# Kernel optimization log

Measured on AMD Instinct MI355X. Metric: run time of the kernel, lower is better.

Reference implementation:

```python
import jax, jax.numpy as jnp
import numpy as np

T, D, F, E, K = 2048, 512, 2048, 8, 2


def setup_inputs() -> dict:
    key = jax.random.key(0)
    ks = jax.random.split(key, 5)
    scaled = lambda k, shape, fan: jax.random.normal(k, shape, jnp.float32) * (fan ** -0.5)
    x = jax.random.normal(ks[0], (T, D), jnp.float32)
    Wg = scaled(ks[1], (D, E), D)          # gate: Linear(D -> E), no bias
    W1 = scaled(ks[2], (E, D, F), D)       # per-expert up proj
    W3 = scaled(ks[3], (E, D, F), D)       # per-expert gate proj (SwiGLU)
    W2 = scaled(ks[4], (E, F, D), F)       # per-expert down proj
    return {"x": x, "Wg": Wg, "W1": W1, "W2": W2, "W3": W3}


def reference(x, Wg, W1, W2, W3):
    # gate logits + top-k routing (topk over raw logits, softmax over the k picked logits,
    # computed in float32 then cast back -- matches the torch source)
    logits = x @ Wg                                   # [T, E]
    topw, sel = jax.lax.top_k(logits, K)              # [T, K] each
    weights = jax.nn.softmax(topw.astype(jnp.float32), axis=-1).astype(x.dtype)
    out = jnp.zeros_like(x)
    # NOTE: the source uses `output[batch_idx] = ...` (assignment, not +=), so later
    # experts OVERWRITE earlier ones for tokens routed to multiple experts.
    # We replicate that exactly with sequential jnp.where overwrites.
    for i in range(E):
        hit = sel == i                                # [T, K]
        mask = hit.any(axis=-1)                       # [T] tokens routed to expert i
        w_i = jnp.sum(jnp.where(hit, weights, 0.0), axis=-1)  # [T] routing weight
        h = jax.nn.silu(x @ W1[i]) * (x @ W3[i])      # [T, F] SwiGLU
        y = h @ W2[i]                                 # [T, D]
        out = jnp.where(mask[:, None], w_i[:, None] * y, out)
    return out
```

## Files before the change

kernel.cpp:

```cpp
#include <hip/hip_runtime.h>
#include <hip/hip_bf16.h>
#include <math.h>

typedef __attribute__((ext_vector_type(8))) short short8;
typedef __attribute__((ext_vector_type(4))) float f32x4;

#define T_TOK 2048
#define D_DIM 512
#define F_DIM 2048
#define E_NUM 8
#define MAXT1 40

__device__ __forceinline__ unsigned short f2bf(float f) {
  union { float f; unsigned u; } c; c.f = f;
  unsigned u = c.u;
  return (unsigned short)((u + 0x7fffu + ((u >> 16) & 1u)) >> 16);
}

__device__ __forceinline__ void gld16(const void* g, void* l) {
  __builtin_amdgcn_global_load_lds((const __attribute__((address_space(1))) int*)g,
                                   (__attribute__((address_space(3))) int*)l, 16, 0, 0);
}

__global__ __launch_bounds__(256) void k_prep(const float* __restrict__ xin,
                                              const float* __restrict__ Wg,
                                              const float* __restrict__ W1,
                                              const float* __restrict__ W3,
                                              int* __restrict__ jbuf,
                                              float* __restrict__ wbuf,
                                              unsigned short* __restrict__ xb,
                                              unsigned short* __restrict__ w1f,
                                              unsigned short* __restrict__ w3f) {
  __shared__ float4 tile4[64 * 32];
  int bz = blockIdx.x, tid = threadIdx.x;

  if (bz < 256) {
    int gid = bz * 256 + tid;
    int t = gid >> 5, seg = gid & 31;
    const float* xp = xin + (size_t)t * D_DIM + seg * 16;
    unsigned short* xo = xb + (size_t)t * D_DIM + seg * 16;
    float acc[8];
#pragma unroll
    for (int e = 0; e < 8; ++e) acc[e] = 0.f;
#pragma unroll
    for (int i = 0; i < 4; ++i) {
      float4 v = *(const float4*)(xp + i * 4);
      ushort4 o;
      o.x = f2bf(v.x); o.y = f2bf(v.y); o.z = f2bf(v.z); o.w = f2bf(v.w);
      *(ushort4*)(xo + i * 4) = o;
      const float* xs = (const float*)&v;
#pragma unroll
      for (int q = 0; q < 4; ++q) {
        int d = seg * 16 + i * 4 + q;
        const float4* wr = (const float4*)(Wg + (size_t)d * 8);
        float4 w0 = wr[0], w1 = wr[1];
        acc[0] += xs[q] * w0.x; acc[1] += xs[q] * w0.y;
        acc[2] += xs[q] * w0.z; acc[3] += xs[q] * w0.w;
        acc[4] += xs[q] * w1.x; acc[5] += xs[q] * w1.y;
        acc[6] += xs[q] * w1.z; acc[7] += xs[q] * w1.w;
      }
    }
#pragma unroll
    for (int off = 1; off < 32; off <<= 1)
#pragma unroll
      for (int e = 0; e < 8; ++e) acc[e] += __shfl_xor(acc[e], off);
    if (seg == 0) {
      float l0 = -1e30f, l1 = -1e30f; int i0 = 0, i1 = 0;
#pragma unroll
      for (int e = 0; e < 8; ++e) {
        float l = acc[e];
        if (l > l0) { l1 = l0; i1 = i0; l0 = l; i0 = e; }
        else if (l > l1) { l1 = l; i1 = e; }
      }
      int j; float w;
      if (i0 > i1) { j = i0; w = 1.f / (1.f + expf(l1 - l0)); }
      else         { j = i1; w = 1.f / (1.f + expf(l0 - l1)); }
      jbuf[t] = j; wbuf[t] = w;
    }
    return;
  }

  int idx = bz - 256;
  int z = idx >> 7, rem = idx & 127;
  const int K = 512, N = 2048;
  int n0 = (rem & 15) * 128, k0 = (rem >> 4) * 64;
  size_t zsz = (size_t)(K / 32) * (N / 16) * 512;
  const float* in; unsigned short* out;
  if (z < 8) { in = W1 + (size_t)z * K * N;       out = w1f + (size_t)z * zsz; }
  else       { in = W3 + (size_t)(z - 8) * K * N; out = w3f + (size_t)(z - 8) * zsz; }
  {
    int lr = tid >> 5, lc = tid & 31;
#pragma unroll
    for (int it = 0; it < 8; ++it) {
      int row = it * 8 + lr;
      float4 v = *(const float4*)(in + (size_t)(k0 + row) * N + n0 + lc * 4);
      tile4[row * 32 + ((lc + (row >> 3) * 4) & 31)] = v;
    }
  }
  __syncthreads();
  const float* tf = (const float*)tile4;
  int wv = tid >> 6, l = tid & 63;
  int n4l = (l & 15) >> 2, nr = l & 3, kg = (l >> 4) * 8;
#pragma unroll
  for (int q = 0; q < 4; ++q) {
    int fid = wv * 4 + q;
    int nb = fid >> 1, kb = fid & 1;
    int n4 = nb * 4 + n4l;
    short8 o;
#pragma unroll
    for (int j = 0; j < 8; ++j) {
      int k = kb * 32 + kg + j;
      int slot = k * 32 + ((n4 + (k >> 3) * 4) & 31);
      o[j] = (short)f2bf(tf[slot * 4 + nr]);
    }
    unsigned short* op = out + (((size_t)(n0 / 16 + nb) * (K / 32)) + (k0 / 32 + kb)) * 512 + l * 8;
    *(short8*)op = o;
  }
}

__global__ __launch_bounds__(256) void k_bucket(const int* __restrict__ jbuf,
                                                int* __restrict__ cntp,
                                                int* __restrict__ basep,
                                                int* __restrict__ list,
                                                int* __restrict__ tl1,
                                                int* __restrict__ ntl) {
  __shared__ int scnt[8], scur[8];
  int tid = threadIdx.x;
  if (tid < 8) scnt[tid] = 0;
  __syncthreads();
  for (int t = tid; t < T_TOK; t += 256) atomicAdd(&scnt[jbuf[t]], 1);
  __syncthreads();
  if (tid == 0) {
    int run = 0;
    for (int e = 0; e < 8; ++e) {
      cntp[e] = scnt[e]; basep[e] = run; scur[e] = run;
      run += scnt[e];
    }
    int n1 = 0, bb = 0;
    for (int e = 0; e < 8; ++e) {
      for (int m = 0; m < scnt[e]; m += 64) tl1[n1++] = (e << 16) | (bb + m);
      bb += scnt[e];
    }
    ntl[0] = n1;
  }
  __syncthreads();
  for (int t = tid; t < T_TOK; t += 256) {
    int j = jbuf[t];
    int p = atomicAdd(&scur[j], 1);
    list[p] = t;
  }
}

__global__ __launch_bounds__(256, 2) void k_ffn1w2(const unsigned short* __restrict__ xb,
                                                   const unsigned short* __restrict__ w1f,
                                                   const unsigned short* __restrict__ w3f,
                                                   const float* __restrict__ W2,
                                                   unsigned short* __restrict__ w2f,
                                                   const int* __restrict__ cntp,
                                                   const int* __restrict__ basep,
                                                   const int* __restrict__ list,
                                                   const int* __restrict__ tl1,
                                                   const int* __restrict__ ntl,
                                                   unsigned short* __restrict__ hbuf) {
  __shared__ unsigned short sA[64 * 512];
  int tid = threadIdx.x, wv = tid >> 6, l = tid & 63;

  if (blockIdx.x >= 640) {
    int idx = blockIdx.x - 640;
    int z = idx >> 7, rem = idx & 127;
    const int K = 2048, N = 512;
    int n0 = (rem & 3) * 128, k0 = (rem >> 2) * 64;
    size_t zsz = (size_t)(K / 32) * (N / 16) * 512;
    const float* in = W2 + (size_t)z * K * N;
    unsigned short* out = w2f + (size_t)z * zsz;
    float4* tile4 = (float4*)sA;
    {
      int lr = tid >> 5, lc = tid & 31;
#pragma unroll
      for (int it = 0; it < 8; ++it) {
        int row = it * 8 + lr;
        float4 v = *(const float4*)(in + (size_t)(k0 + row) * N + n0 + lc * 4);
        tile4[row * 32 + ((lc + (row >> 3) * 4) & 31)] = v;
      }
    }
    __syncthreads();
    const float* tf = (const float*)tile4;
    int n4l = (l & 15) >> 2, nr = l & 3, kg = (l >> 4) * 8;
#pragma unroll
    for (int q = 0; q < 4; ++q) {
      int fid = wv * 4 + q;
      int nb = fid >> 1, kb = fid & 1;
      int n4 = nb * 4 + n4l;
      short8 o;
#pragma unroll
      for (int j = 0; j < 8; ++j) {
        int k = kb * 32 + kg + j;
        int slot = k * 32 + ((n4 + (k >> 3) * 4) & 31);
        o[j] = (short)f2bf(tf[slot * 4 + nr]);
      }
      unsigned short* op = out + (((size_t)(n0 / 16 + nb) * (K / 32)) + (k0 / 32 + kb)) * 512 + l * 8;
      *(short8*)op = o;
    }
    return;
  }

  int L = blockIdx.x;
  int b = (L & 7) * 80 + (L >> 3);
  int x = b % 40, y = b / 40;
  if (x >= ntl[0]) return;
  int pk = tl1[x];
  int e = pk >> 16, g0 = pk & 0xffff;
  int lim = basep[e] + cntp[e];
  int wr = wv >> 1, wc = wv & 1;

#pragma unroll
  for (int it = 0; it < 16; ++it) {
    int row = wv * 16 + it;
    int gr = g0 + row; if (gr >= lim) gr = lim - 1;
    int tok = list[gr];
    int slot = (l & 56) | ((l & 7) ^ (row & 7));
    gld16(xb + (size_t)tok * D_DIM + slot * 8, sA + row * 512);
  }

  const unsigned short* w1b = w1f + ((size_t)(e * 128 + y * 8 + wc) * 16) * 512 + l * 8;
  const unsigned short* w3b = w3f + ((size_t)(e * 128 + y * 8 + wc) * 16) * 512 + l * 8;

  short8 P1[8], P3[8], Q1[8], Q3[8];
  auto loadS = [&](short8* r1, short8* r3, int s) {
    int g = s >> 1, h = s & 1;
    const unsigned short* p1 = w1b + ((size_t)(g * 32 + h * 8)) * 512;
    const unsigned short* p3 = w3b + ((size_t)(g * 32 + h * 8)) * 512;
#pragma unroll
    for (int q = 0; q < 8; ++q) {
      r1[q] = *(const short8*)(p1 + (size_t)q * 512);
      r3[q] = *(const short8*)(p3 + (size_t)q * 512);
    }
  };

  f32x4 au[2], av[2];
  auto halfC = [&](const short8* r1, const short8* r3, int h) {
#pragma unroll
    for (int q = 0; q < 8; ++q) {
      int kf = h * 8 + q;
      short8 a[2];
#pragma unroll
      for (int i = 0; i < 2; ++i) {
        int r = wr * 32 + i * 16 + (l & 15);
        int slot = kf * 4 + (l >> 4);
        int swz = (slot & 56) | ((slot & 7) ^ (r & 7));
        a[i] = *(const short8*)(sA + r * 512 + swz * 8);
      }
#pragma unroll
      for (int i = 0; i < 2; ++i) {
        au[i] = __builtin_amdgcn_mfma_f32_16x16x32_bf16(a[i], r1[q], au[i], 0, 0, 0);
        av[i] = __builtin_amdgcn_mfma_f32_16x16x32_bf16(a[i], r3[q], av[i], 0, 0, 0);
      }
    }
  };

  loadS(P1, P3, 0);
  __syncthreads();

  int cloc = l & 15, rb = (l >> 4) * 4;
#pragma unroll
  for (int gp = 0; gp < 4; ++gp) {
#pragma unroll
    for (int i = 0; i < 2; ++i) {
      au[i] = (f32x4){0.f, 0.f, 0.f, 0.f};
      av[i] = (f32x4){0.f, 0.f, 0.f, 0.f};
    }
    loadS(Q1, Q3, gp * 2 + 1);
    halfC(P1, P3, 0);
    if (gp < 3) loadS(P1, P3, gp * 2 + 2);
    halfC(Q1, Q3, 1);
    int col = (y * 4 + gp) * 32 + wc * 16 + cloc;
#pragma unroll
    for (int i = 0; i < 2; ++i)
#pragma unroll
      for (int r = 0; r < 4; ++r) {
        int gr = g0 + wr * 32 + i * 16 + rb + r;
        if (gr < lim) {
          float uu = au[i][r], vv = av[i][r];
          float hh = (uu / (1.f + expf(-uu))) * vv;
          hbuf[(size_t)gr * F_DIM + col] = f2bf(hh);
        }
      }
  }
}

__global__ __launch_bounds__(256, 3) void k_ffn2(const unsigned short* __restrict__ hbuf,
                                                 const unsigned short* __restrict__ w2f,
                                                 const int* __restrict__ cntp,
                                                 const int* __restrict__ basep,
                                                 const int* __restrict__ list,
                                                 const int* __restrict__ tl1,
                                                 const int* __restrict__ ntl,
                                                 const float* __restrict__ wbuf,
                                                 float* __restrict__ out) {
  int L = blockIdx.x;
  int c = L & 7, q = L >> 3;
  int x = c * 5 + (q % 5);
  int nt = q / 5;
  if (x >= ntl[0]) return;
  int pk = tl1[x];
  int e = pk >> 16, g0 = pk & 0xffff;
  int lim = basep[e] + cntp[e];
  __shared__ unsigned short sA[2 * 8192];
  int tid = threadIdx.x, wv = tid >> 6, l = tid & 63;
  int wr = wv >> 1, wc = wv & 1;

  auto stage = [&](int buf, int ck) {
#pragma unroll
    for (int it = 0; it < 4; ++it) {
      int row0 = it * 16 + wv * 4;
      int row = row0 + (l >> 4);
      int gr = g0 + row; if (gr > T_TOK - 1) gr = T_TOK - 1;
      int sl = (l & 8) | ((l & 7) ^ (row & 7));
      gld16(hbuf + (size_t)gr * F_DIM + ck * 128 + sl * 8, sA + buf * 8192 + row0 * 128);
    }
  };

  const unsigned short* b2p = w2f + ((size_t)(e * 32 + nt * 2 + wc) * 64) * 512 + l * 8;

  short8 Ba[4], Bb[4];
  auto loadB = [&](short8* B, int ck) {
#pragma unroll
    for (int kk = 0; kk < 4; ++kk)
      B[kk] = *(const short8*)(b2p + (size_t)(ck * 4 + kk) * 512);
  };

  f32x4 acc[2];
  acc[0] = (f32x4){0.f, 0.f, 0.f, 0.f};
  acc[1] = (f32x4){0.f, 0.f, 0.f, 0.f};

  auto compute = [&](const short8* B, int cur) {
#pragma unroll
    for (int kk = 0; kk < 4; ++kk) {
      short8 a[2];
#pragma unroll
      for (int i = 0; i < 2; ++i) {
        int r = wr * 32 + i * 16 + (l & 15);
        int slot = kk * 4 + (l >> 4);
        int swz = (slot & 8) | ((slot & 7) ^ (r & 7));
        a[i] = *(const short8*)(sA + cur * 8192 + r * 128 + swz * 8);
      }
      acc[0] = __builtin_amdgcn_mfma_f32_16x16x32_bf16(a[0], B[kk], acc[0], 0, 0, 0);
      acc[1] = __builtin_amdgcn_mfma_f32_16x16x32_bf16(a[1], B[kk], acc[1], 0, 0, 0);
    }
  };

  stage(0, 0);
  loadB(Ba, 0);
  __syncthreads();
  int cur = 0;
  for (int ck = 0; ck < 16; ck += 2) {
    stage(cur ^ 1, ck + 1);
    loadB(Bb, ck + 1);
    compute(Ba, cur);
    __syncthreads();
    cur ^= 1;
    if (ck + 2 < 16) {
      stage(cur ^ 1, ck + 2);
      loadB(Ba, ck + 2);
    }
    compute(Bb, cur);
    __syncthreads();
    cur ^= 1;
  }

  int cloc = l & 15, rb = (l >> 4) * 4;
#pragma unroll
  for (int i = 0; i < 2; ++i)
#pragma unroll
    for (int r = 0; r < 4; ++r) {
      int gr = g0 + wr * 32 + i * 16 + rb + r;
      if (gr < lim) {
        int tok = list[gr];
        out[(size_t)tok * D_DIM + nt * 32 + wc * 16 + cloc] = wbuf[tok] * acc[i][r];
      }
    }
}

extern "C" void kernel_launch(void* const* d_in, const int* in_sizes, int n_in,
                              void* d_out, int out_size, void* d_ws, size_t ws_size,
                              hipStream_t stream) {
  const float* x  = (const float*)d_in[0];
  const float* Wg = (const float*)d_in[1];
  const float* W1 = (const float*)d_in[2];
  const float* W2 = (const float*)d_in[3];
  const float* W3 = (const float*)d_in[4];
  float* out = (float*)d_out;
  char* ws = (char*)d_ws;

  int*            jbuf  = (int*)(ws + 0);
  float*          wbuf  = (float*)(ws + 8192);
  int*            cntp  = (int*)(ws + 16384);
  int*            basep = (int*)(ws + 16448);
  int*            list  = (int*)(ws + 16640);
  int*            tl1   = (int*)(ws + 24832);
  int*            ntl   = (int*)(ws + 25600);
  unsigned short* xb    = (unsigned short*)(ws + 32768);
  unsigned short* w1f   = (unsigned short*)(ws + 32768 + 2097152);
  unsigned short* w3f   = (unsigned short*)(ws + 32768 + 2097152 + 16777216);
  unsigned short* w2f   = (unsigned short*)(ws + 32768 + 2097152 + 2 * 16777216);
  unsigned short* hbuf  = (unsigned short*)(ws + 32768 + 2097152 + 3 * 16777216);

  k_prep<<<dim3(2304), dim3(256), 0, stream>>>(x, Wg, W1, W3, jbuf, wbuf, xb, w1f, w3f);
  k_bucket<<<dim3(1), dim3(256), 0, stream>>>(jbuf, cntp, basep, list, tl1, ntl);
  k_ffn1w2<<<dim3(1664), dim3(256), 0, stream>>>(xb, w1f, w3f, W2, w2f, cntp, basep, list, tl1, ntl, hbuf);
  k_ffn2<<<dim3(640), dim3(256), 0, stream>>>(hbuf, w2f, cntp, basep, list, tl1, ntl, wbuf, out);
}
```

Before: 79.82 us.

## Split routing kernel, fuse bucketing into weight prep, double-buffer weight conversion tiles

Routing and x-to-bf16 conversion move into their own kernel. The single-block bucketing kernel is folded in as an extra block of the W1/W3 conversion kernel, so bucketing runs alongside weight conversion instead of as a separate serial launch. Each weight-conversion block now handles two 64-row k tiles with a double-buffered LDS tile, which halves the block count and overlaps the next tile's loads with the current tile's conversion and stores. The cost is more LDS per block in prep2, which may lower occupancy.

```diff
diff --git a/kernel.cpp b/kernel.cpp
--- a/kernel.cpp
+++ b/kernel.cpp
@@ -22,133 +22,141 @@
                                    (__attribute__((address_space(3))) int*)l, 16, 0, 0);
 }
 
-__global__ __launch_bounds__(256) void k_prep(const float* __restrict__ xin,
-                                              const float* __restrict__ Wg,
-                                              const float* __restrict__ W1,
-                                              const float* __restrict__ W3,
-                                              int* __restrict__ jbuf,
-                                              float* __restrict__ wbuf,
-                                              unsigned short* __restrict__ xb,
-                                              unsigned short* __restrict__ w1f,
-                                              unsigned short* __restrict__ w3f) {
-  __shared__ float4 tile4[64 * 32];
+__global__ __launch_bounds__(256) void k_route(const float* __restrict__ xin,
+                                               const float* __restrict__ Wg,
+                                               int* __restrict__ jbuf,
+                                               float* __restrict__ wbuf,
+                                               unsigned short* __restrict__ xb) {
+  int gid = blockIdx.x * 256 + threadIdx.x;
+  int t = gid >> 5, seg = gid & 31;
+  const float* xp = xin + (size_t)t * D_DIM + seg * 16;
+  unsigned short* xo = xb + (size_t)t * D_DIM + seg * 16;
+  float acc[8];
+#pragma unroll
+  for (int e = 0; e < 8; ++e) acc[e] = 0.f;
+#pragma unroll
+  for (int i = 0; i < 4; ++i) {
+    float4 v = *(const float4*)(xp + i * 4);
+    ushort4 o;
+    o.x = f2bf(v.x); o.y = f2bf(v.y); o.z = f2bf(v.z); o.w = f2bf(v.w);
+    *(ushort4*)(xo + i * 4) = o;
+    const float* xs = (const float*)&v;
+#pragma unroll
+    for (int q = 0; q < 4; ++q) {
+      int d = seg * 16 + i * 4 + q;
+      const float4* wr = (const float4*)(Wg + (size_t)d * 8);
+      float4 w0 = wr[0], w1 = wr[1];
+      acc[0] += xs[q] * w0.x; acc[1] += xs[q] * w0.y;
+      acc[2] += xs[q] * w0.z; acc[3] += xs[q] * w0.w;
+      acc[4] += xs[q] * w1.x; acc[5] += xs[q] * w1.y;
+      acc[6] += xs[q] * w1.z; acc[7] += xs[q] * w1.w;
+    }
+  }
+#pragma unroll
+  for (int off = 1; off < 32; off <<= 1)
+#pragma unroll
+    for (int e = 0; e < 8; ++e) acc[e] += __shfl_xor(acc[e], off);
+  if (seg == 0) {
+    float l0 = -1e30f, l1 = -1e30f; int i0 = 0, i1 = 0;
+#pragma unroll
+    for (int e = 0; e < 8; ++e) {
+      float l = acc[e];
+      if (l > l0) { l1 = l0; i1 = i0; l0 = l; i0 = e; }
+      else if (l > l1) { l1 = l; i1 = e; }
+    }
+    int j; float w;
+    if (i0 > i1) { j = i0; w = 1.f / (1.f + expf(l1 - l0)); }
+    else         { j = i1; w = 1.f / (1.f + expf(l0 - l1)); }
+    jbuf[t] = j; wbuf[t] = w;
+  }
+}
+
+__global__ __launch_bounds__(256) void k_prep2(const float* __restrict__ W1,
+                                               const float* __restrict__ W3,
+                                               unsigned short* __restrict__ w1f,
+                                               unsigned short* __restrict__ w3f,
+                                               const int* __restrict__ jbuf,
+                                               int* __restrict__ cntp,
+                                               int* __restrict__ basep,
+                                               int* __restrict__ list,
+                                               int* __restrict__ tl1,
+                                               int* __restrict__ ntl) {
+  __shared__ float4 tile4[2][64 * 32];
+  __shared__ int scnt[8], scur[8];
   int bz = blockIdx.x, tid = threadIdx.x;
 
-  if (bz < 256) {
-    int gid = bz * 256 + tid;
-    int t = gid >> 5, seg = gid & 31;
-    const float* xp = xin + (size_t)t * D_DIM + seg * 16;
-    unsigned short* xo = xb + (size_t)t * D_DIM + seg * 16;
-    float acc[8];
-#pragma unroll
-    for (int e = 0; e < 8; ++e) acc[e] = 0.f;
-#pragma unroll
-    for (int i = 0; i < 4; ++i) {
-      float4 v = *(const float4*)(xp + i * 4);
-      ushort4 o;
-      o.x = f2bf(v.x); o.y = f2bf(v.y); o.z = f2bf(v.z); o.w = f2bf(v.w);
-      *(ushort4*)(xo + i * 4) = o;
-      const float* xs = (const float*)&v;
-#pragma unroll
-      for (int q = 0; q < 4; ++q) {
-        int d = seg * 16 + i * 4 + q;
-        const float4* wr = (const float4*)(Wg + (size_t)d * 8);
-        float4 w0 = wr[0], w1 = wr[1];
-        acc[0] += xs[q] * w0.x; acc[1] += xs[q] * w0.y;
-        acc[2] += xs[q] * w0.z; acc[3] += xs[q] * w0.w;
-        acc[4] += xs[q] * w1.x; acc[5] += xs[q] * w1.y;
-        acc[6] += xs[q] * w1.z; acc[7] += xs[q] * w1.w;
-      }
-    }
-#pragma unroll
-    for (int off = 1; off < 32; off <<= 1)
-#pragma unroll
-      for (int e = 0; e < 8; ++e) acc[e] += __shfl_xor(acc[e], off);
-    if (seg == 0) {
-      float l0 = -1e30f, l1 = -1e30f; int i0 = 0, i1 = 0;
-#pragma unroll
+  if (bz >= 1024) {
+    if (tid < 8) scnt[tid] = 0;
+    __syncthreads();
+    for (int t = tid; t < T_TOK; t += 256) atomicAdd(&scnt[jbuf[t]], 1);
+    __syncthreads();
+    if (tid == 0) {
+      int run = 0;
       for (int e = 0; e < 8; ++e) {
-        float l = acc[e];
-        if (l > l0) { l1 = l0; i1 = i0; l0 = l; i0 = e; }
-        else if (l > l1) { l1 = l; i1 = e; }
-      }
-      int j; float w;
-      if (i0 > i1) { j = i0; w = 1.f / (1.f + expf(l1 - l0)); }
-      else         { j = i1; w = 1.f / (1.f + expf(l0 - l1)); }
-      jbuf[t] = j; wbuf[t] = w;
+        cntp[e] = scnt[e]; basep[e] = run; scur[e] = run;
+        run += scnt[e];
+      }
+      int n1 = 0, bb = 0;
+      for (int e = 0; e < 8; ++e) {
+        for (int m = 0; m < scnt[e]; m += 64) tl1[n1++] = (e << 16) | (bb + m);
+        bb += scnt[e];
+      }
+      ntl[0] = n1;
+    }
+    __syncthreads();
+    for (int t = tid; t < T_TOK; t += 256) {
+      int j = jbuf[t];
+      int p = atomicAdd(&scur[j], 1);
+      list[p] = t;
     }
     return;
   }
 
-  int idx = bz - 256;
-  int z = idx >> 7, rem = idx & 127;
+  int z = bz >> 6, rem = bz & 63;
   const int K = 512, N = 2048;
-  int n0 = (rem & 15) * 128, k0 = (rem >> 4) * 64;
+  int n0 = (rem & 15) * 128, k0 = (rem >> 4) * 128;
   size_t zsz = (size_t)(K / 32) * (N / 16) * 512;
   const float* in; unsigned short* out;
   if (z < 8) { in = W1 + (size_t)z * K * N;       out = w1f + (size_t)z * zsz; }
   else       { in = W3 + (size_t)(z - 8) * K * N; out = w3f + (size_t)(z - 8) * zsz; }
-  {
-    int lr = tid >> 5, lc = tid & 31;
+
+  int lr = tid >> 5, lc = tid & 31;
+  int wv = tid >> 6, l = tid & 63;
+  int n4l = (l & 15) >> 2, nr = l & 3, kg = (l >> 4) * 8;
+
+  auto loadT = [&](int buf, int kb0) {
 #pragma unroll
     for (int it = 0; it < 8; ++it) {
       int row = it * 8 + lr;
-      float4 v = *(const float4*)(in + (size_t)(k0 + row) * N + n0 + lc * 4);
-      tile4[row * 32 + ((lc + (row >> 3) * 4) & 31)] = v;
-    }
-  }
+      float4 v = *(const float4*)(in + (size_t)(kb0 + row) * N + n0 + lc * 4);
+      tile4[buf][row * 32 + ((lc + (row >> 3) * 4) & 31)] = v;
+    }
+  };
+  auto storeT = [&](int buf, int kb0) {
+    const float* tf = (const float*)&tile4[buf][0];
+#pragma unroll
+    for (int q = 0; q < 4; ++q) {
+      int fid = wv * 4 + q;
+      int nb = fid >> 1, kb = fid & 1;
+      int n4 = nb * 4 + n4l;
+      short8 o;
+#pragma unroll
+      for (int j = 0; j < 8; ++j) {
+        int k = kb * 32 + kg + j;
+        int slot = k * 32 + ((n4 + (k >> 3) * 4) & 31);
+        o[j] = (short)f2bf(tf[slot * 4 + nr]);
+      }
+      unsigned short* op = out + (((size_t)(n0 / 16 + nb) * (K / 32)) + (kb0 / 32 + kb)) * 512 + l * 8;
+      *(short8*)op = o;
+    }
+  };
+
+  loadT(0, k0);
   __syncthreads();
-  const float* tf = (const float*)tile4;
-  int wv = tid >> 6, l = tid & 63;
-  int n4l = (l & 15) >> 2, nr = l & 3, kg = (l >> 4) * 8;
-#pragma unroll
-  for (int q = 0; q < 4; ++q) {
-    int fid = wv * 4 + q;
-    int nb = fid >> 1, kb = fid & 1;
-    int n4 = nb * 4 + n4l;
-    short8 o;
-#pragma unroll
-    for (int j = 0; j < 8; ++j) {
-      int k = kb * 32 + kg + j;
-      int slot = k * 32 + ((n4 + (k >> 3) * 4) & 31);
-      o[j] = (short)f2bf(tf[slot * 4 + nr]);
-    }
-    unsigned short* op = out + (((size_t)(n0 / 16 + nb) * (K / 32)) + (k0 / 32 + kb)) * 512 + l * 8;
-    *(short8*)op = o;
-  }
-}
-
-__global__ __launch_bounds__(256) void k_bucket(const int* __restrict__ jbuf,
-                                                int* __restrict__ cntp,
-                                                int* __restrict__ basep,
-                                                int* __restrict__ list,
-                                                int* __restrict__ tl1,
-                                                int* __restrict__ ntl) {
-  __shared__ int scnt[8], scur[8];
-  int tid = threadIdx.x;
-  if (tid < 8) scnt[tid] = 0;
+  loadT(1, k0 + 64);
+  storeT(0, k0);
   __syncthreads();
-  for (int t = tid; t < T_TOK; t += 256) atomicAdd(&scnt[jbuf[t]], 1);
-  __syncthreads();
-  if (tid == 0) {
-    int run = 0;
-    for (int e = 0; e < 8; ++e) {
-      cntp[e] = scnt[e]; basep[e] = run; scur[e] = run;
-      run += scnt[e];
-    }
-    int n1 = 0, bb = 0;
-    for (int e = 0; e < 8; ++e) {
-      for (int m = 0; m < scnt[e]; m += 64) tl1[n1++] = (e << 16) | (bb + m);
-      bb += scnt[e];
-    }
-    ntl[0] = n1;
-  }
-  __syncthreads();
-  for (int t = tid; t < T_TOK; t += 256) {
-    int j = jbuf[t];
-    int p = atomicAdd(&scur[j], 1);
-    list[p] = t;
-  }
+  storeT(1, k0 + 64);
 }
 
 __global__ __launch_bounds__(256, 2) void k_ffn1w2(const unsigned short* __restrict__ xb,
@@ -162,45 +170,55 @@
                                                    const int* __restrict__ tl1,
                                                    const int* __restrict__ ntl,
                                                    unsigned short* __restrict__ hbuf) {
-  __shared__ unsigned short sA[64 * 512];
+  __shared__ __align__(16) unsigned short sA[64 * 512];
   int tid = threadIdx.x, wv = tid >> 6, l = tid & 63;
 
   if (blockIdx.x >= 640) {
     int idx = blockIdx.x - 640;
-    int z = idx >> 7, rem = idx & 127;
+    int z = idx >> 6, rem = idx & 63;
     const int K = 2048, N = 512;
-    int n0 = (rem & 3) * 128, k0 = (rem >> 2) * 64;
+    int n0 = (rem & 3) * 128, k0 = (rem >> 2) * 128;
     size_t zsz = (size_t)(K / 32) * (N / 16) * 512;
     const float* in = W2 + (size_t)z * K * N;
     unsigned short* out = w2f + (size_t)z * zsz;
     float4* tile4 = (float4*)sA;
-    {
-      int lr = tid >> 5, lc = tid & 31;
+
+    int lr = tid >> 5, lc = tid & 31;
+    int n4l = (l & 15) >> 2, nr = l & 3, kg = (l >> 4) * 8;
+
+    auto loadT = [&](int buf, int kb0) {
 #pragma unroll
       for (int it = 0; it < 8; ++it) {
         int row = it * 8 + lr;
-        float4 v = *(const float4*)(in + (size_t)(k0 + row) * N + n0 + lc * 4);
-        tile4[row * 32 + ((lc + (row >> 3) * 4) & 31)] = v;
-      }
-    }
-    __syncthreads();
-    const float* tf = (const float*)tile4;
-    int n4l = (l & 15) >> 2, nr = l & 3, kg = (l >> 4) * 8;
-#pragma unroll
-    for (int q = 0; q < 4; ++q) {
-      int fid = wv * 4 + q;
-      int nb = fid >> 1, kb = fid & 1;
-      int n4 = nb * 4 + n4l;
-      short8 o;
-#pragma unroll
-      for (int j = 0; j < 8; ++j) {
-        int k = kb * 32 + kg + j;
-        int slot = k * 32 + ((n4 + (k >> 3) * 4) & 31);
-        o[j] = (short)f2bf(tf[slot * 4 + nr]);
-      }
-      unsigned short* op = out + (((size_t)(n0 / 16 + nb) * (K / 32)) + (k0 / 32 + kb)) * 512 + l * 8;
-      *(short8*)op = o;
-    }
+        float4 v = *(const float4*)(in + (size_t)(kb0 + row) * N + n0 + lc * 4);
+        tile4[buf * 2048 + row * 32 + ((lc + (row >> 3) * 4) & 31)] = v;
+      }
+    };
+    auto storeT = [&](int buf, int kb0) {
+      const float* tf = (const float*)&tile4[buf * 2048];
+#pragma unroll
+      for (int q = 0; q < 4; ++q) {
+        int fid = wv * 4 + q;
+        int nb = fid >> 1, kb = fid & 1;
+        int n4 = nb * 4 + n4l;
+        short8 o;
+#pragma unroll
+        for (int j = 0; j < 8; ++j) {
+          int k = kb * 32 + kg + j;
+          int slot = k * 32 + ((n4 + (k >> 3) * 4) & 31);
+          o[j] = (short)f2bf(tf[slot * 4 + nr]);
+        }
+        unsigned short* op = out + (((size_t)(n0 / 16 + nb) * (K / 32)) + (kb0 / 32 + kb)) * 512 + l * 8;
+        *(short8*)op = o;
+      }
+    };
+
+    loadT(0, k0);
+    __syncthreads();
+    loadT(1, k0 + 64);
+    storeT(0, k0);
+    __syncthreads();
+    storeT(1, k0 + 64);
     return;
   }
 
@@ -405,8 +423,8 @@
   unsigned short* w2f   = (unsigned short*)(ws + 32768 + 2097152 + 2 * 16777216);
   unsigned short* hbuf  = (unsigned short*)(ws + 32768 + 2097152 + 3 * 16777216);
 
-  k_prep<<<dim3(2304), dim3(256), 0, stream>>>(x, Wg, W1, W3, jbuf, wbuf, xb, w1f, w3f);
-  k_bucket<<<dim3(1), dim3(256), 0, stream>>>(jbuf, cntp, basep, list, tl1, ntl);
-  k_ffn1w2<<<dim3(1664), dim3(256), 0, stream>>>(xb, w1f, w3f, W2, w2f, cntp, basep, list, tl1, ntl, hbuf);
+  k_route<<<dim3(256), dim3(256), 0, stream>>>(x, Wg, jbuf, wbuf, xb);
+  k_prep2<<<dim3(1025), dim3(256), 0, stream>>>(W1, W3, w1f, w3f, jbuf, cntp, basep, list, tl1, ntl);
+  k_ffn1w2<<<dim3(1152), dim3(256), 0, stream>>>(xb, w1f, w3f, W2, w2f, cntp, basep, list, tl1, ntl, hbuf);
   k_ffn2<<<dim3(640), dim3(256), 0, stream>>>(hbuf, w2f, cntp, basep, list, tl1, ntl, wbuf, out);
 }
```

Measured after the change: 80.19 us. Within noise of the previous version (+0.5%).
